# Performance work log

Hardware: AMD Instinct MI355X
Metric: run time of the kernel (lower is better)

The kernel has to match this reference:

```python
import jax, jax.numpy as jnp
import numpy as np

D_MODEL = 512
NHEAD = 8
MAX_REL = 256  # max_relative_position


def _linear(x, w, b):
    # torch nn.Linear: y = x @ W^T + b, W: [out, in]
    return jnp.einsum('...i,oi->...o', x, w) + b


def setup_inputs() -> dict:
    key = jax.random.key(0)
    ks = jax.random.split(key, 16)
    B, S, D = 32, 512, D_MODEL
    s = 0.02
    inp = {
        'query': jax.random.normal(ks[0], (B, S, D), jnp.float32),
        'key':   jax.random.normal(ks[1], (B, S, D), jnp.float32),
        'value': jax.random.normal(ks[2], (B, S, D), jnp.float32),
        # local attention projections (torch Linear weights [out,in])
        'wq': jax.random.normal(ks[3], (D, D), jnp.float32) * s,
        'bq': jnp.zeros((D,), jnp.float32),
        'wk': jax.random.normal(ks[4], (D, D), jnp.float32) * s,
        'bk': jnp.zeros((D,), jnp.float32),
        'wv': jax.random.normal(ks[5], (D, D), jnp.float32) * s,
        'bv': jnp.zeros((D,), jnp.float32),
        'wo': jax.random.normal(ks[6], (D, D), jnp.float32) * s,
        'bo': jnp.zeros((D,), jnp.float32),
        # relative-position key embedding table [2*MAX_REL+1, head_dim]
        'rel_k': jax.random.normal(ks[7], (2 * MAX_REL + 1, D // NHEAD), jnp.float32) * s,
        # global nn.MultiheadAttention (nhead//2 heads): packed in_proj + out_proj
        'g_in_w': jax.random.normal(ks[8], (3 * D, D), jnp.float32) * s,
        'g_in_b': jnp.zeros((3 * D,), jnp.float32),
        'g_out_w': jax.random.normal(ks[9], (D, D), jnp.float32) * s,
        'g_out_b': jnp.zeros((D,), jnp.float32),
    }
    return inp


def reference(query, key, value, wq, bq, wk, bk, wv, bv, wo, bo, rel_k,
              g_in_w, g_in_b, g_out_w, g_out_b):
    B, S, D = query.shape
    H, hd = NHEAD, D // NHEAD

    # --- local attention with relative-position bias ---
    q = _linear(query, wq, bq).reshape(B, S, H, hd).transpose(0, 2, 1, 3)  # [B,H,S,hd]
    k = _linear(key,   wk, bk).reshape(B, S, H, hd).transpose(0, 2, 1, 3)
    v = _linear(value, wv, bv).reshape(B, S, H, hd).transpose(0, 2, 1, 3)

    scores = jnp.einsum('bhqd,bhkd->bhqk', q, k) / jnp.sqrt(jnp.float32(hd))

    # relative positions: distance[i,j] = j - i, clamped, shifted to [0, 2*MAX_REL]
    idx = jnp.arange(S)
    rel_ids = jnp.clip(idx[None, :] - idx[:, None], -MAX_REL, MAX_REL) + MAX_REL  # [S,S]
    rel_pos_k = rel_k[rel_ids]  # [S, S, hd]
    scores = scores + jnp.einsum('bhld,lrd->bhlr', q, rel_pos_k)

    attn = jax.nn.softmax(scores, axis=-1)
    local = jnp.einsum('bhqk,bhkd->bhqd', attn, v)
    local = local.transpose(0, 2, 1, 3).reshape(B, S, D)

    # --- global MHA with H//2 heads ---
    Hg = H // 2
    hdg = D // Hg
    qg = _linear(query, g_in_w[:D], g_in_b[:D]).reshape(B, S, Hg, hdg).transpose(0, 2, 1, 3)
    kg = _linear(key,   g_in_w[D:2 * D], g_in_b[D:2 * D]).reshape(B, S, Hg, hdg).transpose(0, 2, 1, 3)
    vg = _linear(value, g_in_w[2 * D:], g_in_b[2 * D:]).reshape(B, S, Hg, hdg).transpose(0, 2, 1, 3)
    gs = jnp.einsum('bhqd,bhkd->bhqk', qg, kg) / jnp.sqrt(jnp.float32(hdg))
    ga = jax.nn.softmax(gs, axis=-1)
    g = jnp.einsum('bhqk,bhkd->bhqd', ga, vg).transpose(0, 2, 1, 3).reshape(B, S, D)
    g = _linear(g, g_out_w, g_out_b)

    combined = 0.7 * local + 0.3 * g
    return _linear(combined, wo, bo)
```

## Files before the change

kernel.cpp:

```cpp
#include <hip/hip_runtime.h>

typedef __attribute__((ext_vector_type(8))) short bh8;
typedef __attribute__((ext_vector_type(4))) float f4;

#define DEVI static __device__ __forceinline__

DEVI unsigned short f2b(float f) {
  union { float f; unsigned u; } v; v.f = f;
  unsigned r = v.u + 0x7fffu + ((v.u >> 16) & 1u);
  return (unsigned short)(r >> 16);
}
DEVI float b2f(unsigned short h) {
  union { unsigned u; float f; } v; v.u = ((unsigned)h) << 16;
  return v.f;
}
DEVI f4 mfma16(bh8 a, bh8 b, f4 c) {
  return __builtin_amdgcn_mfma_f32_16x16x32_bf16(a, b, c, 0, 0, 0);
}
DEVI void gload_lds16(const unsigned short* g, unsigned short* l) {
  __builtin_amdgcn_global_load_lds(
      (const __attribute__((address_space(1))) void*)(g),
      (__attribute__((address_space(3))) void*)(l), 16, 0, 0);
}

__global__ __launch_bounds__(256) void prep_x_kern(
    const float* __restrict__ q, const float* __restrict__ k, const float* __restrict__ v,
    unsigned short* __restrict__ xq, unsigned short* __restrict__ xk, unsigned short* __restrict__ xv) {
  long i = ((long)blockIdx.x * 256 + threadIdx.x) * 4;
  if (i >= 8388608L) return;
  float4 a = *(const float4*)(q + i);
  float4 b = *(const float4*)(k + i);
  float4 c = *(const float4*)(v + i);
  union { unsigned short s[4]; uint2 u; } pa, pb, pc;
  pa.s[0] = f2b(a.x); pa.s[1] = f2b(a.y); pa.s[2] = f2b(a.z); pa.s[3] = f2b(a.w);
  pb.s[0] = f2b(b.x); pb.s[1] = f2b(b.y); pb.s[2] = f2b(b.z); pb.s[3] = f2b(b.w);
  pc.s[0] = f2b(c.x); pc.s[1] = f2b(c.y); pc.s[2] = f2b(c.z); pc.s[3] = f2b(c.w);
  *(uint2*)(xq + i) = pa.u;
  *(uint2*)(xk + i) = pb.u;
  *(uint2*)(xv + i) = pc.u;
}

__global__ __launch_bounds__(256) void prep_w_kern(
    const float* __restrict__ wq, const float* __restrict__ wk, const float* __restrict__ wv,
    const float* __restrict__ g_in_w, const float* __restrict__ g_out_w,
    const float* __restrict__ wo, const float* __restrict__ rel_k,
    unsigned short* __restrict__ Wq, unsigned short* __restrict__ Wk, unsigned short* __restrict__ Wv,
    unsigned short* __restrict__ Wo_, unsigned short* __restrict__ WgoT,
    unsigned short* __restrict__ Bfin, unsigned short* __restrict__ Rk) {
  long i = ((long)blockIdx.x * 256 + threadIdx.x) * 4;
  if (i >= 2392128L) return;
  if (i >= 2097152L && i < 2359296L) {
    long off = i - 2097152L;
    int ii = (int)(off >> 9), p = (int)(off & 511);
    union { unsigned short s[4]; uint2 u; } w;
#pragma unroll
    for (int tt = 0; tt < 4; tt++) w.s[tt] = f2b(g_out_w[(p + tt) * 512 + ii]);
    *(uint2*)(WgoT + off) = w.u;
    return;
  }
  const float* src; unsigned short* dst; long off; float sc = 1.0f;
  if (i < 524288L)        { dst = Wq;  off = i; src = (i < 262144L) ? wq + i : g_in_w + (i - 262144L); }
  else if (i < 1048576L)  { long j = i - 524288L;  dst = Wk;  off = j; src = (j < 262144L) ? wk + j : g_in_w + j; }
  else if (i < 1572864L)  { long j = i - 1048576L; dst = Wv;  off = j; src = (j < 262144L) ? wv + j : g_in_w + 262144L + j; }
  else if (i < 1835008L)  { long j = i - 1572864L; dst = Wo_; off = j; src = wo + j; }
  else if (i < 2097152L)  { long j = i - 1835008L; int col = (int)(j >> 9), k = (int)(j & 511);
                            dst = Bfin; off = (long)col * 1024 + k; src = wo + j; sc = 0.7f; }
  else                    { long j = i - 2359296L; dst = Rk;  off = j; src = rel_k + j; }
  float4 f = *(const float4*)src;
  union { unsigned short s[4]; uint2 u; } p;
  p.s[0] = f2b(f.x * sc); p.s[1] = f2b(f.y * sc); p.s[2] = f2b(f.z * sc); p.s[3] = f2b(f.w * sc);
  *(uint2*)(dst + off) = p.u;
}

__global__ __launch_bounds__(256) void bias2_kern(
    const float* __restrict__ wo, const float* __restrict__ bgo,
    const float* __restrict__ bo, float* __restrict__ bias2) {
  int o = blockIdx.x * 256 + threadIdx.x;
  if (o >= 512) return;
  const float* r = wo + (long)o * 512;
  float s = 0.f;
#pragma unroll 4
  for (int m = 0; m < 512; m += 4) {
    float4 a = *(const float4*)(r + m);
    float4 b = *(const float4*)(bgo + m);
    s += a.x * b.x + a.y * b.y + a.z * b.z + a.w * b.w;
  }
  bias2[o] = bo[o] + 0.3f * s;
}

template <int NB, int EPI, int KD, int LDA, int GRIDM>
__global__ __launch_bounds__(256) void gemm_bf16_kern(
    const unsigned short* __restrict__ A, const unsigned short* __restrict__ Bw,
    const float* __restrict__ bias0, const float* __restrict__ bias1,
    unsigned short* __restrict__ outb, unsigned short* __restrict__ outb2,
    float* __restrict__ outf) {
  __shared__ unsigned short lsA[128 * 32];
  __shared__ unsigned short lsB[128 * 32];
  const int t = threadIdx.x;
  const int lane = t & 63, w = t >> 6;
  const int l15 = lane & 15, g8 = (lane >> 4) * 8, g4 = (lane >> 4) * 4;
  int n = blockIdx.x;
  int rb, cb;
  if constexpr (GRIDM > 0) {
    rb = (n % GRIDM) * 128; cb = (n / GRIDM) * 128;
  } else {
    int x = n >> 3, c = n & 7;
    rb = (c * 16 + (x & 15)) * 128;
    cb = (x >> 4) * 128;
  }
  const int wr = (w >> 1) * 64, wc = (w & 1) * 64;
  const int e0 = t * 8, e1 = 2048 + t * 8;
  const int r0 = e0 >> 5, k0i = e0 & 31;
  const int r1 = e1 >> 5, k1i = e1 & 31;

  const unsigned short* pa0 = A + (long)(rb + r0) * LDA + k0i;
  const unsigned short* pa1 = A + (long)(rb + r1) * LDA + k1i;
  const unsigned short* pb0 = Bw + (long)(cb + r0) * KD + k0i;
  const unsigned short* pb1 = Bw + (long)(cb + r1) * KD + k1i;
  unsigned short* dA0 = lsA + w * 512;
  unsigned short* dA1 = lsA + 2048 + w * 512;
  unsigned short* dB0 = lsB + w * 512;
  unsigned short* dB1 = lsB + 2048 + w * 512;

  f4 acc[4][4] = {};
  for (int k0 = 0; k0 < KD; k0 += 32) {
    __syncthreads();
    gload_lds16(pa0 + k0, dA0);
    gload_lds16(pa1 + k0, dA1);
    gload_lds16(pb0 + k0, dB0);
    gload_lds16(pb1 + k0, dB1);
    __syncthreads();
    bh8 af[4], bf[4];
#pragma unroll
    for (int m = 0; m < 4; m++) af[m] = *(const bh8*)(lsA + (wr + m * 16 + l15) * 32 + g8);
#pragma unroll
    for (int nn = 0; nn < 4; nn++) bf[nn] = *(const bh8*)(lsB + (wc + nn * 16 + l15) * 32 + g8);
#pragma unroll
    for (int m = 0; m < 4; m++)
#pragma unroll
      for (int nn = 0; nn < 4; nn++)
        acc[m][nn] = mfma16(af[m], bf[nn], acc[m][nn]);
  }
#pragma unroll
  for (int m = 0; m < 4; m++) {
#pragma unroll
    for (int nn = 0; nn < 4; nn++) {
      if constexpr (EPI == 3) {
        int col = cb + wc + nn * 16 + l15;
        float bsv = (col < 512) ? bias0[col] : bias1[col - 512];
        unsigned r[4];
#pragma unroll
        for (int j = 0; j < 4; j++) {
          union { float f; unsigned u; } v; v.f = acc[m][nn][j] + bsv;
          r[j] = v.u + 0x7fffu + ((v.u >> 16) & 1u);
        }
        unsigned lo = (r[0] >> 16) | (r[1] & 0xffff0000u);
        unsigned hi = (r[2] >> 16) | (r[3] & 0xffff0000u);
        int row0 = rb + wr + m * 16 + g4;
        int bb = row0 >> 9, s = row0 & 511;
        if (col < 512) {
          int hh = col >> 6, d = col & 63;
          *(uint2*)(outb + (((long)(bb * 8 + hh) * 64 + d) << 9) + s) = make_uint2(lo, hi);
        } else {
          int c2 = col - 512, hg = c2 >> 7, dg = c2 & 127;
          *(uint2*)(outb2 + (((long)(bb * 4 + hg) * 128 + dg) << 9) + s) = make_uint2(lo, hi);
        }
      } else {
#pragma unroll
        for (int j = 0; j < 4; j++) {
          int row = rb + wr + m * 16 + g4 + j;
          int col = cb + wc + nn * 16 + l15;
          float v = acc[m][nn][j];
          if constexpr (EPI == 0) {
            v += (col < 512) ? bias0[col] : bias1[col - 512];
            outb[(long)row * (NB * 128) + col] = f2b(v);
          } else if constexpr (EPI == 5) {
            outb[(long)row * 1024 + 512 + col] = f2b(0.3f * v);
          } else {
            v += bias0[col];
            outf[(long)row * 512 + col] = v;
          }
        }
      }
    }
  }
}

__global__ __launch_bounds__(512, 4) void attn_local_kern(
    const unsigned short* __restrict__ Yq, const unsigned short* __restrict__ Yk,
    const unsigned short* __restrict__ Yvt, const unsigned short* __restrict__ relk,
    unsigned short* __restrict__ outC) {
  __shared__ unsigned short kv[2][8192];
  __shared__ unsigned short buf[32 * 524];
  __shared__ float redbuf[8][32];

  const int t = threadIdx.x, lane = t & 63, w = t >> 6;
  const int l15 = lane & 15, g = lane >> 4, g8 = g * 8;
  int n = blockIdx.x;
  int bid = (n & 7) * 512 + (n >> 3);
  const int qt = bid & 15;
  const int h = (bid >> 4) & 7;
  const int b = bid >> 7;
  const int qb = qt * 32;
  const long base = ((long)(b * 512)) * 1024 + h * 64;
  const long vbase = ((long)(b * 8 + h)) * 64 * 512;

#define STAGE_K(ROFF, BUF) { \
    const int c_ = t & 7; \
    _Pragma("unroll") \
    for (int it = 0; it < 2; it++) { \
      int rr = it * 64 + (t >> 3); \
      gload_lds16(Yk + base + (long)((ROFF) + rr) * 1024 + ((c_ ^ (rr & 7)) * 8), \
                  kv[BUF] + it * 4096 + w * 512); \
    } }
#define STAGE_V(COFF, BUF) { \
    const int c_ = t & 15; \
    _Pragma("unroll") \
    for (int it = 0; it < 2; it++) { \
      int dd_ = it * 32 + (t >> 4); \
      gload_lds16(Yvt + vbase + (long)dd_ * 512 + (COFF) + ((c_ ^ (dd_ & 15)) * 8), \
                  kv[BUF] + it * 4096 + w * 512); \
    } }
#define QK(CH) { \
    int rl = w * 16 + l15; \
    const unsigned short* kb_ = kv[(CH) & 1]; \
    bh8 k0 = *(const bh8*)(kb_ + rl * 64 + ((g ^ (rl & 7)) * 8)); \
    bh8 k1 = *(const bh8*)(kb_ + rl * 64 + (((g + 4) ^ (rl & 7)) * 8)); \
    _Pragma("unroll") \
    for (int mm = 0; mm < 2; mm++) { \
      f4 a = {}; \
      a = mfma16(qf[mm][0], k0, a); \
      a = mfma16(qf[mm][1], k1, a); \
      sc[mm][CH] = a; \
    } }
#define GATHER(CH) { \
    _Pragma("unroll") \
    for (int mm = 0; mm < 2; mm++) \
    _Pragma("unroll") \
    for (int j = 0; j < 4; j++) { \
      int lr = mm * 16 + g * 4 + j; \
      int rowb = lr * 524; \
      int idx = rowb + 256 - (qb + lr) + (CH) * 128 + w * 16 + l15; \
      idx = idx < rowb ? rowb : idx; \
      idx = idx > rowb + 512 ? rowb + 512 : idx; \
      float p = exp2f(fmaf(sc[mm][CH][j], 0.18033688011112042f, b2f(buf[idx]))); \
      sc[mm][CH][j] = p; \
      rs[mm][j] += p; \
    } }

  STAGE_K(0, 0);

  bh8 qf[2][2];
#pragma unroll
  for (int mm = 0; mm < 2; mm++) {
    const unsigned short* qp = Yq + base + (long)(qb + mm * 16 + l15) * 1024 + g8;
    qf[mm][0] = *(const bh8*)(qp);
    qf[mm][1] = *(const bh8*)(qp + 32);
  }

  for (int tt = w; tt < 33; tt += 8) {
    int ri = tt * 16 + l15; if (ri > 512) ri = 512;
    const unsigned short* rp = relk + ri * 64 + g8;
    bh8 rf0 = *(const bh8*)(rp), rf1 = *(const bh8*)(rp + 32);
    int col = tt * 16 + l15;
#pragma unroll
    for (int mm = 0; mm < 2; mm++) {
      f4 a = {};
      a = mfma16(qf[mm][0], rf0, a);
      a = mfma16(qf[mm][1], rf1, a);
      if (col < 524) {
#pragma unroll
        for (int j = 0; j < 4; j++)
          buf[(mm * 16 + g * 4 + j) * 524 + col] = f2b(a[j] * 1.4426950408889634f);
      }
    }
  }
  __syncthreads();

  f4 sc[2][4];
  float rs[2][4] = {};

#pragma unroll
  for (int c = 0; c < 4; c++) {
    if (c < 3) { STAGE_K((c + 1) * 128, (c + 1) & 1); }
    else       { STAGE_V(0, 0); }
    __builtin_amdgcn_s_setprio(1);
    QK(c);
    __builtin_amdgcn_s_setprio(0);
    GATHER(c);
    __syncthreads();
  }

#pragma unroll
  for (int mm = 0; mm < 2; mm++)
#pragma unroll
    for (int j = 0; j < 4; j++) {
      int lr = mm * 16 + g * 4 + j;
      float s = rs[mm][j];
      for (int d = 1; d < 16; d <<= 1) s += __shfl_xor(s, d, 64);
      if (l15 == 0) redbuf[w][lr] = s;
    }
#pragma unroll
  for (int mm = 0; mm < 2; mm++)
#pragma unroll
    for (int ch = 0; ch < 4; ch++) {
      int col = ch * 128 + w * 16 + l15;
#pragma unroll
      for (int j = 0; j < 4; j++)
        buf[(mm * 16 + g * 4 + j) * 524 + col] = f2b(sc[mm][ch][j]);
    }
  __syncthreads();

  const int mmw = w >> 2, dt = w & 3;
  const int dd = dt * 16 + l15;
  float rinvj[4];
#pragma unroll
  for (int j = 0; j < 4; j++) {
    int lr = mmw * 16 + g * 4 + j;
    float s = 0.f;
#pragma unroll
    for (int ww = 0; ww < 8; ww++) s += redbuf[ww][lr];
    rinvj[j] = __builtin_amdgcn_rcpf(s);
  }

  f4 accO = {};
#pragma unroll
  for (int d = 0; d < 4; d++) {
    if (d < 3) { STAGE_V((d + 1) * 128, (d + 1) & 1); }
    const unsigned short* vb_ = kv[d & 1];
    __builtin_amdgcn_s_setprio(1);
#pragma unroll
    for (int ks2 = 0; ks2 < 4; ks2++) {
      union { uint2 u[2]; bh8 v; } pa;
      const unsigned short* pp = buf + (mmw * 16 + l15) * 524 + (d * 4 + ks2) * 32 + g8;
      pa.u[0] = *(const uint2*)(pp);
      pa.u[1] = *(const uint2*)(pp + 4);
      bh8 vv = *(const bh8*)(vb_ + dd * 128 + (((ks2 * 4 + g) ^ (dd & 15)) * 8));
      accO = mfma16(pa.v, vv, accO);
    }
    __builtin_amdgcn_s_setprio(0);
    if (d < 3) __syncthreads();
  }
#pragma unroll
  for (int j = 0; j < 4; j++) {
    int row = qb + mmw * 16 + g * 4 + j;
    outC[((long)(b * 512 + row)) * 1024 + h * 64 + dt * 16 + l15] = f2b(accO[j] * rinvj[j]);
  }
#undef STAGE_K
#undef STAGE_V
#undef QK
#undef GATHER
}

__global__ __launch_bounds__(512) void attn_glob_kern(
    const unsigned short* __restrict__ Yq, const unsigned short* __restrict__ Yk,
    const unsigned short* __restrict__ Yvt, unsigned short* __restrict__ outC) {
  __shared__ unsigned short buf[32 * 520];
  __shared__ float redbuf[8][32];

  const int t = threadIdx.x, lane = t & 63, w = t >> 6;
  const int l15 = lane & 15, g = lane >> 4, g8 = g * 8;
  int n = blockIdx.x;
  int bid = (n & 7) * 256 + (n >> 3);
  const int qt = bid & 15;
  const int hg = (bid >> 4) & 3;
  const int b = bid >> 6;
  const int qb = qt * 32;
  const long base = ((long)(b * 512)) * 1024 + 512 + hg * 128;

  bh8 qf[2][4];
#pragma unroll
  for (int mm = 0; mm < 2; mm++) {
    const unsigned short* qp = Yq + base + (long)(qb + mm * 16 + l15) * 1024 + g8;
#pragma unroll
    for (int ks = 0; ks < 4; ks++) qf[mm][ks] = *(const bh8*)(qp + ks * 32);
  }

  f4 sc[2][4];
  __builtin_amdgcn_s_setprio(1);
#pragma unroll
  for (int ct = 0; ct < 4; ct++) {
    int r = w * 64 + ct * 16 + l15;
    const unsigned short* kp = Yk + base + (long)r * 1024 + g8;
    bh8 kf[4];
#pragma unroll
    for (int ks = 0; ks < 4; ks++) kf[ks] = *(const bh8*)(kp + ks * 32);
#pragma unroll
    for (int mm = 0; mm < 2; mm++) {
      f4 a = {};
#pragma unroll
      for (int ks = 0; ks < 4; ks++) a = mfma16(qf[mm][ks], kf[ks], a);
      sc[mm][ct] = a;
    }
  }
  __builtin_amdgcn_s_setprio(0);

#pragma unroll
  for (int mm = 0; mm < 2; mm++) {
#pragma unroll
    for (int j = 0; j < 4; j++) {
      int lr = mm * 16 + g * 4 + j;
      float s = 0.f;
#pragma unroll
      for (int ct = 0; ct < 4; ct++) {
        float p = exp2f(sc[mm][ct][j] * 0.12751745334f);
        sc[mm][ct][j] = p;
        s += p;
      }
      for (int d = 1; d < 16; d <<= 1) s += __shfl_xor(s, d, 64);
      if (l15 == 0) redbuf[w][lr] = s;
    }
  }
#pragma unroll
  for (int mm = 0; mm < 2; mm++)
#pragma unroll
    for (int ct = 0; ct < 4; ct++) {
      int col = w * 64 + ct * 16 + l15;
#pragma unroll
      for (int j = 0; j < 4; j++)
        buf[(mm * 16 + g * 4 + j) * 520 + col] = f2b(sc[mm][ct][j]);
    }
  __syncthreads();

  float rinv[2][4];
#pragma unroll
  for (int mm = 0; mm < 2; mm++)
#pragma unroll
    for (int j = 0; j < 4; j++) {
      int lr = mm * 16 + g * 4 + j;
      float s = 0.f;
#pragma unroll
      for (int ww = 0; ww < 8; ww++) s += redbuf[ww][lr];
      rinv[mm][j] = __builtin_amdgcn_rcpf(s);
    }

  f4 accO[2] = {};
  const unsigned short* vr = Yvt + ((long)(b * 4 + hg) * 128 + w * 16 + l15) * 512;
  __builtin_amdgcn_s_setprio(1);
#pragma unroll
  for (int ks = 0; ks < 16; ks++) {
    bh8 vb = *(const bh8*)(vr + ks * 32 + g8);
#pragma unroll
    for (int mm = 0; mm < 2; mm++) {
      union { uint2 u[2]; bh8 v; } pa;
      const unsigned short* pp = buf + (mm * 16 + l15) * 520 + ks * 32 + g8;
      pa.u[0] = *(const uint2*)(pp);
      pa.u[1] = *(const uint2*)(pp + 4);
      accO[mm] = mfma16(pa.v, vb, accO[mm]);
    }
  }
  __builtin_amdgcn_s_setprio(0);
#pragma unroll
  for (int mm = 0; mm < 2; mm++)
#pragma unroll
    for (int j = 0; j < 4; j++) {
      int row = qb + mm * 16 + g * 4 + j;
      outC[((long)(b * 512 + row)) * 1024 + 512 + hg * 128 + w * 16 + l15] = f2b(accO[mm][j] * rinv[mm][j]);
    }
}

extern "C" void kernel_launch(void* const* d_in, const int* in_sizes, int n_in,
                              void* d_out, int out_size, void* d_ws, size_t ws_size,
                              hipStream_t stream) {
  const float* query = (const float*)d_in[0];
  const float* key   = (const float*)d_in[1];
  const float* value = (const float*)d_in[2];
  const float* wq = (const float*)d_in[3];   const float* bq = (const float*)d_in[4];
  const float* wk = (const float*)d_in[5];   const float* bk = (const float*)d_in[6];
  const float* wv = (const float*)d_in[7];   const float* bv = (const float*)d_in[8];
  const float* wo = (const float*)d_in[9];   const float* bo = (const float*)d_in[10];
  const float* rel_k = (const float*)d_in[11];
  const float* g_in_w = (const float*)d_in[12];  const float* g_in_b = (const float*)d_in[13];
  const float* g_out_w = (const float*)d_in[14]; const float* g_out_b = (const float*)d_in[15];

  unsigned short* p = (unsigned short*)d_ws;
  unsigned short* Xq = p;            p += 8388608;
  unsigned short* Xk = p;            p += 8388608;
  unsigned short* Xv = p;            p += 8388608;
  unsigned short* Yq = p;            p += 16777216;
  unsigned short* Yk = p;            p += 16777216;
  unsigned short* Yvt_l = p;         p += 8388608;
  unsigned short* Yvt_g = p;         p += 8388608;
  unsigned short* Wq = p;            p += 524288;
  unsigned short* Wk = p;            p += 524288;
  unsigned short* Wv = p;            p += 524288;
  unsigned short* Wo_ = p;           p += 262144;
  unsigned short* WgoT = p;          p += 262144;
  unsigned short* Bfin = p;          p += 524288;
  unsigned short* Rk = p;            p += 32832;
  float* bias2 = (float*)p;          p += 1024;
  unsigned short* CAT = Xq;

  prep_x_kern<<<8192, 256, 0, stream>>>(query, key, value, Xq, Xk, Xv);
  prep_w_kern<<<2337, 256, 0, stream>>>(wq, wk, wv, g_in_w, g_out_w, wo, rel_k,
                                        Wq, Wk, Wv, Wo_, WgoT, Bfin, Rk);
  bias2_kern<<<2, 256, 0, stream>>>(wo, g_out_b, bo, bias2);

  gemm_bf16_kern<4, 5, 512, 512, 4><<<16, 256, 0, stream>>>(
      Wo_, WgoT, nullptr, nullptr, Bfin, nullptr, nullptr);

  gemm_bf16_kern<8, 0, 512, 512, 0><<<1024, 256, 0, stream>>>(Xq, Wq, bq, g_in_b, Yq, nullptr, nullptr);
  gemm_bf16_kern<8, 0, 512, 512, 0><<<1024, 256, 0, stream>>>(Xk, Wk, bk, g_in_b + 512, Yk, nullptr, nullptr);
  gemm_bf16_kern<8, 3, 512, 512, 0><<<1024, 256, 0, stream>>>(Xv, Wv, bv, g_in_b + 1024, Yvt_l, Yvt_g, nullptr);

  attn_local_kern<<<4096, 512, 0, stream>>>(Yq, Yk, Yvt_l, Rk, CAT);
  attn_glob_kern<<<2048, 512, 0, stream>>>(Yq, Yk, Yvt_g, CAT);

  gemm_bf16_kern<4, 2, 1024, 1024, 0><<<512, 256, 0, stream>>>(
      CAT, Bfin, bias2, nullptr, nullptr, nullptr, (float*)d_out);
}
```

Before: 361.1 us.

## Double-buffer GEMM LDS loads and fold small prep kernels into larger launches

The GEMM main loop now double-buffers its LDS tiles: the next k-slice is issued into the alternate buffer while MFMAs run on the current one, using one barrier per iteration instead of two, and MFMA priority is raised with s_setprio. The bias2 reduction moves into extra blocks of prep_w_kern, and the small Wo·WgoT weight-fold GEMM becomes 16 extra blocks of the Q projection GEMM, removing two launches. The cost is double the LDS per block, which may lower occupancy, plus some extra branching in the GEMM kernel.

```diff
diff --git a/kernel.cpp b/kernel.cpp
--- a/kernel.cpp
+++ b/kernel.cpp
@@ -44,9 +44,26 @@
     const float* __restrict__ wq, const float* __restrict__ wk, const float* __restrict__ wv,
     const float* __restrict__ g_in_w, const float* __restrict__ g_out_w,
     const float* __restrict__ wo, const float* __restrict__ rel_k,
+    const float* __restrict__ bgo, const float* __restrict__ bo,
     unsigned short* __restrict__ Wq, unsigned short* __restrict__ Wk, unsigned short* __restrict__ Wv,
     unsigned short* __restrict__ Wo_, unsigned short* __restrict__ WgoT,
-    unsigned short* __restrict__ Bfin, unsigned short* __restrict__ Rk) {
+    unsigned short* __restrict__ Bfin, unsigned short* __restrict__ Rk,
+    float* __restrict__ bias2) {
+  if (blockIdx.x >= 2337) {
+    int o = (blockIdx.x - 2337) * 256 + threadIdx.x;
+    if (o < 512) {
+      const float* r = wo + (long)o * 512;
+      float s = 0.f;
+#pragma unroll 4
+      for (int m = 0; m < 512; m += 4) {
+        float4 a = *(const float4*)(r + m);
+        float4 b = *(const float4*)(bgo + m);
+        s += a.x * b.x + a.y * b.y + a.z * b.z + a.w * b.w;
+      }
+      bias2[o] = bo[o] + 0.3f * s;
+    }
+    return;
+  }
   long i = ((long)blockIdx.x * 256 + threadIdx.x) * 4;
   if (i >= 2392128L) return;
   if (i >= 2097152L && i < 2359296L) {
@@ -72,34 +89,20 @@
   *(uint2*)(dst + off) = p.u;
 }
 
-__global__ __launch_bounds__(256) void bias2_kern(
-    const float* __restrict__ wo, const float* __restrict__ bgo,
-    const float* __restrict__ bo, float* __restrict__ bias2) {
-  int o = blockIdx.x * 256 + threadIdx.x;
-  if (o >= 512) return;
-  const float* r = wo + (long)o * 512;
-  float s = 0.f;
-#pragma unroll 4
-  for (int m = 0; m < 512; m += 4) {
-    float4 a = *(const float4*)(r + m);
-    float4 b = *(const float4*)(bgo + m);
-    s += a.x * b.x + a.y * b.y + a.z * b.z + a.w * b.w;
-  }
-  bias2[o] = bo[o] + 0.3f * s;
-}
-
-template <int NB, int EPI, int KD, int LDA, int GRIDM>
+template <int NB, int EPI, int KD, int LDA, int GRIDM, int W2JOB>
 __global__ __launch_bounds__(256) void gemm_bf16_kern(
     const unsigned short* __restrict__ A, const unsigned short* __restrict__ Bw,
     const float* __restrict__ bias0, const float* __restrict__ bias1,
     unsigned short* __restrict__ outb, unsigned short* __restrict__ outb2,
-    float* __restrict__ outf) {
-  __shared__ unsigned short lsA[128 * 32];
-  __shared__ unsigned short lsB[128 * 32];
+    float* __restrict__ outf,
+    const unsigned short* __restrict__ A2, const unsigned short* __restrict__ B2) {
+  __shared__ unsigned short lsA[2][4096];
+  __shared__ unsigned short lsB[2][4096];
   const int t = threadIdx.x;
   const int lane = t & 63, w = t >> 6;
   const int l15 = lane & 15, g8 = (lane >> 4) * 8, g4 = (lane >> 4) * 4;
   int n = blockIdx.x;
+  bool w2 = false;
   int rb, cb;
   if constexpr (GRIDM > 0) {
     rb = (n % GRIDM) * 128; cb = (n / GRIDM) * 128;
@@ -108,38 +111,70 @@
     rb = (c * 16 + (x & 15)) * 128;
     cb = (x >> 4) * 128;
   }
+  const unsigned short* Ap = A;
+  const unsigned short* Bp = Bw;
+  if constexpr (W2JOB) {
+    if (n >= 1024) {
+      w2 = true;
+      int m2 = n - 1024;
+      rb = (m2 & 3) * 128; cb = (m2 >> 2) * 128;
+      Ap = A2; Bp = B2;
+    }
+  }
   const int wr = (w >> 1) * 64, wc = (w & 1) * 64;
   const int e0 = t * 8, e1 = 2048 + t * 8;
   const int r0 = e0 >> 5, k0i = e0 & 31;
   const int r1 = e1 >> 5, k1i = e1 & 31;
 
-  const unsigned short* pa0 = A + (long)(rb + r0) * LDA + k0i;
-  const unsigned short* pa1 = A + (long)(rb + r1) * LDA + k1i;
-  const unsigned short* pb0 = Bw + (long)(cb + r0) * KD + k0i;
-  const unsigned short* pb1 = Bw + (long)(cb + r1) * KD + k1i;
-  unsigned short* dA0 = lsA + w * 512;
-  unsigned short* dA1 = lsA + 2048 + w * 512;
-  unsigned short* dB0 = lsB + w * 512;
-  unsigned short* dB1 = lsB + 2048 + w * 512;
+  const unsigned short* pa0 = Ap + (long)(rb + r0) * LDA + k0i;
+  const unsigned short* pa1 = Ap + (long)(rb + r1) * LDA + k1i;
+  const unsigned short* pb0 = Bp + (long)(cb + r0) * KD + k0i;
+  const unsigned short* pb1 = Bp + (long)(cb + r1) * KD + k1i;
+
+#define GSTAGE(KK, BUF) { \
+    gload_lds16(pa0 + (KK), lsA[BUF] + w * 512); \
+    gload_lds16(pa1 + (KK), lsA[BUF] + 2048 + w * 512); \
+    gload_lds16(pb0 + (KK), lsB[BUF] + w * 512); \
+    gload_lds16(pb1 + (KK), lsB[BUF] + 2048 + w * 512); }
+
+  GSTAGE(0, 0);
+  __syncthreads();
 
   f4 acc[4][4] = {};
+  int cur = 0;
   for (int k0 = 0; k0 < KD; k0 += 32) {
-    __syncthreads();
-    gload_lds16(pa0 + k0, dA0);
-    gload_lds16(pa1 + k0, dA1);
-    gload_lds16(pb0 + k0, dB0);
-    gload_lds16(pb1 + k0, dB1);
-    __syncthreads();
     bh8 af[4], bf[4];
 #pragma unroll
-    for (int m = 0; m < 4; m++) af[m] = *(const bh8*)(lsA + (wr + m * 16 + l15) * 32 + g8);
-#pragma unroll
-    for (int nn = 0; nn < 4; nn++) bf[nn] = *(const bh8*)(lsB + (wc + nn * 16 + l15) * 32 + g8);
+    for (int m = 0; m < 4; m++) af[m] = *(const bh8*)(lsA[cur] + (wr + m * 16 + l15) * 32 + g8);
+#pragma unroll
+    for (int nn = 0; nn < 4; nn++) bf[nn] = *(const bh8*)(lsB[cur] + (wc + nn * 16 + l15) * 32 + g8);
+    if (k0 + 32 < KD) GSTAGE(k0 + 32, cur ^ 1);
+    __builtin_amdgcn_s_setprio(1);
 #pragma unroll
     for (int m = 0; m < 4; m++)
 #pragma unroll
       for (int nn = 0; nn < 4; nn++)
         acc[m][nn] = mfma16(af[m], bf[nn], acc[m][nn]);
+    __builtin_amdgcn_s_setprio(0);
+    __syncthreads();
+    cur ^= 1;
+  }
+#undef GSTAGE
+
+  if constexpr (W2JOB) {
+    if (w2) {
+#pragma unroll
+      for (int m = 0; m < 4; m++)
+#pragma unroll
+        for (int nn = 0; nn < 4; nn++)
+#pragma unroll
+          for (int j = 0; j < 4; j++) {
+            int row = rb + wr + m * 16 + g4 + j;
+            int col = cb + wc + nn * 16 + l15;
+            outb2[(long)row * 1024 + 512 + col] = f2b(0.3f * acc[m][nn][j]);
+          }
+      return;
+    }
   }
 #pragma unroll
   for (int m = 0; m < 4; m++) {
@@ -174,8 +209,6 @@
           if constexpr (EPI == 0) {
             v += (col < 512) ? bias0[col] : bias1[col - 512];
             outb[(long)row * (NB * 128) + col] = f2b(v);
-          } else if constexpr (EPI == 5) {
-            outb[(long)row * 1024 + 512 + col] = f2b(0.3f * v);
           } else {
             v += bias0[col];
             outf[(long)row * 512 + col] = v;
@@ -492,20 +525,20 @@
   unsigned short* CAT = Xq;
 
   prep_x_kern<<<8192, 256, 0, stream>>>(query, key, value, Xq, Xk, Xv);
-  prep_w_kern<<<2337, 256, 0, stream>>>(wq, wk, wv, g_in_w, g_out_w, wo, rel_k,
-                                        Wq, Wk, Wv, Wo_, WgoT, Bfin, Rk);
-  bias2_kern<<<2, 256, 0, stream>>>(wo, g_out_b, bo, bias2);
-
-  gemm_bf16_kern<4, 5, 512, 512, 4><<<16, 256, 0, stream>>>(
-      Wo_, WgoT, nullptr, nullptr, Bfin, nullptr, nullptr);
-
-  gemm_bf16_kern<8, 0, 512, 512, 0><<<1024, 256, 0, stream>>>(Xq, Wq, bq, g_in_b, Yq, nullptr, nullptr);
-  gemm_bf16_kern<8, 0, 512, 512, 0><<<1024, 256, 0, stream>>>(Xk, Wk, bk, g_in_b + 512, Yk, nullptr, nullptr);
-  gemm_bf16_kern<8, 3, 512, 512, 0><<<1024, 256, 0, stream>>>(Xv, Wv, bv, g_in_b + 1024, Yvt_l, Yvt_g, nullptr);
+  prep_w_kern<<<2339, 256, 0, stream>>>(wq, wk, wv, g_in_w, g_out_w, wo, rel_k,
+                                        g_out_b, bo,
+                                        Wq, Wk, Wv, Wo_, WgoT, Bfin, Rk, bias2);
+
+  gemm_bf16_kern<8, 0, 512, 512, 0, 1><<<1040, 256, 0, stream>>>(
+      Xq, Wq, bq, g_in_b, Yq, Bfin, nullptr, Wo_, WgoT);
+  gemm_bf16_kern<8, 0, 512, 512, 0, 0><<<1024, 256, 0, stream>>>(
+      Xk, Wk, bk, g_in_b + 512, Yk, nullptr, nullptr, nullptr, nullptr);
+  gemm_bf16_kern<8, 3, 512, 512, 0, 0><<<1024, 256, 0, stream>>>(
+      Xv, Wv, bv, g_in_b + 1024, Yvt_l, Yvt_g, nullptr, nullptr, nullptr);
 
   attn_local_kern<<<4096, 512, 0, stream>>>(Yq, Yk, Yvt_l, Rk, CAT);
   attn_glob_kern<<<2048, 512, 0, stream>>>(Yq, Yk, Yvt_g, CAT);
 
-  gemm_bf16_kern<4, 2, 1024, 1024, 0><<<512, 256, 0, stream>>>(
-      CAT, Bfin, bias2, nullptr, nullptr, nullptr, (float*)d_out);
-}
+  gemm_bf16_kern<4, 2, 1024, 1024, 0, 0><<<512, 256, 0, stream>>>(
+      CAT, Bfin, bias2, nullptr, nullptr, nullptr, (float*)d_out, nullptr, nullptr);
+}
```

Result: no change. 356.1 us (-1.4%).
